# Optimization experiments

Hardware: AMD Instinct MI355X
Metric: run time of the kernel (lower is better)

Reference implementation:

```python
import jax, jax.numpy as jnp
import numpy as np

NQ = 4   # num qubits
NL = 2   # StronglyEntanglingLayers depth


def _apply_1q(state, U, w):
    # state: (B,2,2,2,2) complex64, U: (2,2) complex64, wire w in [0,NQ)
    state = jnp.moveaxis(state, w + 1, -1)
    state = jnp.einsum('ij,...j->...i', U, state)
    return jnp.moveaxis(state, -1, w + 1)


def _apply_cnot(state, cw, tw):
    # flip target axis on the control=1 slice
    s0 = jnp.take(state, jnp.array([0]), axis=cw + 1)
    s1 = jnp.take(state, jnp.array([1]), axis=cw + 1)
    s1 = jnp.flip(s1, axis=tw + 1)
    return jnp.concatenate([s0, s1], axis=cw + 1)


def _simulate(xq, qw):
    # xq: (B, NQ) angles/pi, qw: (NL, NQ, 3) Rot params
    half = 0.5 * jnp.pi * xq                      # RY(pi*x) half-angles
    c, s = jnp.cos(half), jnp.sin(half)           # (B, NQ)
    # RY on |0> gives [cos(t/2), sin(t/2)]: build product state directly
    state = jnp.stack([c[:, 0], s[:, 0]], axis=-1).astype(jnp.complex64)  # (B,2)
    for w in range(1, NQ):
        q = jnp.stack([c[:, w], s[:, w]], axis=-1).astype(jnp.complex64)
        state = jnp.einsum('b...,bj->b...j', state, q)  # -> (B,2,...,2)

    for l in range(NL):
        for w in range(NQ):
            phi, theta, omega = qw[l, w, 0], qw[l, w, 1], qw[l, w, 2]
            ct = jnp.cos(0.5 * theta)
            st = jnp.sin(0.5 * theta)
            a = 0.5 * (phi + omega)
            b = 0.5 * (phi - omega)
            # PennyLane Rot(phi,theta,omega) = RZ(omega) RY(theta) RZ(phi)
            row0 = jnp.stack([jnp.exp(-1j * a) * ct, -jnp.exp(1j * b) * st])
            row1 = jnp.stack([jnp.exp(-1j * b) * st, jnp.exp(1j * a) * ct])
            U = jnp.stack([row0, row1]).astype(jnp.complex64)
            state = _apply_1q(state, U, w)
        r = l % (NQ - 1) + 1  # default ranges of StronglyEntanglingLayers
        for w in range(NQ):
            state = _apply_cnot(state, w, (w + r) % NQ)

    p = state.real ** 2 + state.imag ** 2  # (B,2,2,2,2) probabilities
    ez = []
    for w in range(NQ):
        axes = tuple(a for a in range(1, NQ + 1) if a != w + 1)
        m = p.sum(axis=axes)               # (B,2) marginal of wire w
        ez.append(m[:, 0] - m[:, 1])       # <PauliZ>
    return jnp.stack(ez, axis=1)           # (B, NQ) float32


def setup_inputs() -> dict:
    key = jax.random.key(0)
    ks = jax.random.split(key, 6)
    N, C, H, W, OUT = 8, 128, 128, 128, 128
    x = jax.random.normal(ks[0], (N, C, H, W), dtype=jnp.float32)
    pre_w = jax.random.normal(ks[1], (NQ, C), dtype=jnp.float32) * (1.0 / np.sqrt(C))
    pre_b = jax.random.normal(ks[2], (NQ,), dtype=jnp.float32) * 0.01
    q_weights = jax.random.normal(ks[3], (NL, NQ, 3), dtype=jnp.float32)
    post_w = jax.random.normal(ks[4], (OUT, NQ), dtype=jnp.float32) * 0.5
    post_b = jax.random.normal(ks[5], (OUT,), dtype=jnp.float32) * 0.01
    return {"x": x, "pre_w": pre_w, "pre_b": pre_b, "q_weights": q_weights,
            "post_w": post_w, "post_b": post_b}


def reference(x, pre_w, pre_b, q_weights, post_w, post_b):
    N, C, H, W = x.shape
    xf = x.transpose(0, 2, 3, 1).reshape(-1, C)      # (N*H*W, C)
    xq = xf @ pre_w.T + pre_b                        # (B, NQ)
    z = _simulate(xq, q_weights)                     # (B, NQ)
    out = z @ post_w.T + post_b                      # (B, OUT)
    return out.reshape(N, H, W, -1).transpose(0, 3, 1, 2)
```

## Files before the change

kernel.cpp:

```cpp
#include <hip/hip_runtime.h>
#include <math.h>

#define NQ   4
#define NL   2
#define CD   128
#define HWSZ 16384
#define OUTC 128

typedef float f4 __attribute__((ext_vector_type(4)));

__global__ void qsetup_kernel(const float* __restrict__ qw, float* __restrict__ A) {
    __shared__ float Ur[16][17];
    __shared__ float Ui[16][17];
    __shared__ float sM[4 * 16 * 16];
    const int tid = threadIdx.x;

    if (tid < 16) {
        float sr[16], si[16];
        #pragma unroll
        for (int k = 0; k < 16; ++k) { sr[k] = (k == tid) ? 1.f : 0.f; si[k] = 0.f; }

        #pragma unroll
        for (int l = 0; l < NL; ++l) {
            #pragma unroll
            for (int w = 0; w < NQ; ++w) {
                float phi = qw[(l * NQ + w) * 3 + 0];
                float th  = qw[(l * NQ + w) * 3 + 1];
                float om  = qw[(l * NQ + w) * 3 + 2];
                float ct = __cosf(0.5f * th), st = __sinf(0.5f * th);
                float a = 0.5f * (phi + om), b = 0.5f * (phi - om);
                float sa, ca, sb, cb;
                __sincosf(a, &sa, &ca);
                __sincosf(b, &sb, &cb);
                float u00r =  ca * ct, u00i = -sa * ct;
                float u01r = -cb * st, u01i = -sb * st;
                float u10r =  cb * st, u10i = -sb * st;
                float u11r =  ca * ct, u11i =  sa * ct;
                const int wm = 1 << (3 - w);
                #pragma unroll
                for (int i = 0; i < 16; ++i) {
                    if (i & wm) continue;
                    int i1 = i | wm;
                    float a0r = sr[i],  a0i = si[i];
                    float a1r = sr[i1], a1i = si[i1];
                    sr[i]  = u00r * a0r - u00i * a0i + u01r * a1r - u01i * a1i;
                    si[i]  = u00r * a0i + u00i * a0r + u01r * a1i + u01i * a1r;
                    sr[i1] = u10r * a0r - u10i * a0i + u11r * a1r - u11i * a1i;
                    si[i1] = u10r * a0i + u10i * a0r + u11r * a1i + u11i * a1r;
                }
            }
            const int r = l % (NQ - 1) + 1;
            #pragma unroll
            for (int w = 0; w < NQ; ++w) {
                const int cm = 1 << (3 - w);
                const int tm = 1 << (3 - ((w + r) % NQ));
                #pragma unroll
                for (int i = 0; i < 16; ++i) {
                    if ((i & cm) && !(i & tm)) {
                        int i1 = i | tm;
                        float t;
                        t = sr[i]; sr[i] = sr[i1]; sr[i1] = t;
                        t = si[i]; si[i] = si[i1]; si[i1] = t;
                    }
                }
            }
        }
        #pragma unroll
        for (int k = 0; k < 16; ++k) { Ur[tid][k] = sr[k]; Ui[tid][k] = si[k]; }
    }
    __syncthreads();

    for (int t = tid; t < 4 * 16 * 16; t += blockDim.x) {
        int w = t >> 8, rem = t & 255, i = rem >> 4, j = rem & 15;
        float acc = 0.f;
        #pragma unroll
        for (int k = 0; k < 16; ++k) {
            float sgn = ((k >> (3 - w)) & 1) ? -1.f : 1.f;
            acc += sgn * (Ur[i][k] * Ur[j][k] + Ui[i][k] * Ui[j][k]);
        }
        sM[t] = acc;
    }
    __syncthreads();

    for (int t = tid; t < 4 * 81; t += blockDim.x) {
        int w = t / 81, j = t % 81;
        int j0 = j / 27, j1 = (j / 9) % 3, j2 = (j / 3) % 3, j3 = j % 3;
        int f =  ((j0 == 2) ? 8 : 0) | ((j1 == 2) ? 4 : 0)
               | ((j2 == 2) ? 2 : 0) | ((j3 == 2) ? 1 : 0);
        int zm = ((j0 == 1) ? 8 : 0) | ((j1 == 1) ? 4 : 0)
               | ((j2 == 1) ? 2 : 0) | ((j3 == 1) ? 1 : 0);
        float acc = 0.f;
        #pragma unroll
        for (int i = 0; i < 16; ++i) {
            float sgn = (__popc(i & zm) & 1) ? -1.f : 1.f;
            acc += sM[(w * 16 + (i ^ f)) * 16 + i] * sgn;
        }
        A[t] = acc * 0.0625f;
    }
}

__global__ __launch_bounds__(256) void qmain_kernel(
    const float* __restrict__ x, const float* __restrict__ pre_w,
    const float* __restrict__ pre_b, const float* __restrict__ A,
    const float* __restrict__ post_w, const float* __restrict__ post_b,
    float* __restrict__ out)
{
    __shared__ float zL[4][4][64];

    const int tid    = threadIdx.x;
    const int blk    = blockIdx.x;
    const int n      = blk >> 6;
    const int hwbase = (blk & 63) * 256;
    const float* xp  = x + (size_t)n * CD * HWSZ + hwbase + tid;

    float a0 = pre_b[0], a1 = pre_b[1], a2 = pre_b[2], a3 = pre_b[3];
    #pragma unroll
    for (int c0 = 0; c0 < CD; c0 += 32) {
        float xv[32];
        #pragma unroll
        for (int j = 0; j < 32; ++j)
            xv[j] = xp[(size_t)(c0 + j) * HWSZ];
        #pragma unroll
        for (int j = 0; j < 32; ++j) {
            const int c = c0 + j;
            a0 = fmaf(xv[j], pre_w[0 * CD + c], a0);
            a1 = fmaf(xv[j], pre_w[1 * CD + c], a1);
            a2 = fmaf(xv[j], pre_w[2 * CD + c], a2);
            a3 = fmaf(xv[j], pre_w[3 * CD + c], a3);
        }
    }

    const float PI = 3.14159265358979323846f;
    float cz0 = __cosf(PI * a0), sx0 = __sinf(PI * a0);
    float cz1 = __cosf(PI * a1), sx1 = __sinf(PI * a1);
    float cz2 = __cosf(PI * a2), sx2 = __sinf(PI * a2);
    float cz3 = __cosf(PI * a3), sx3 = __sinf(PI * a3);

    float g01[9], g23[9];
    {
        float t0[3] = { 1.f, cz0, sx0 }, t1[3] = { 1.f, cz1, sx1 };
        float t2[3] = { 1.f, cz2, sx2 }, t3[3] = { 1.f, cz3, sx3 };
        #pragma unroll
        for (int a = 0; a < 3; ++a)
            #pragma unroll
            for (int b = 0; b < 3; ++b) {
                g01[a * 3 + b] = t0[a] * t1[b];
                g23[a * 3 + b] = t2[a] * t3[b];
            }
    }

    float z0 = 0.f, z1 = 0.f, z2 = 0.f, z3 = 0.f;
    #pragma unroll
    for (int j01 = 0; j01 < 9; ++j01)
        #pragma unroll
        for (int j23 = 0; j23 < 9; ++j23) {
            float g = g01[j01] * g23[j23];
            int j = j01 * 9 + j23;
            z0 = fmaf(A[  0 + j], g, z0);
            z1 = fmaf(A[ 81 + j], g, z1);
            z2 = fmaf(A[162 + j], g, z2);
            z3 = fmaf(A[243 + j], g, z3);
        }

    zL[tid & 3][0][tid >> 2] = z0;
    zL[tid & 3][1][tid >> 2] = z1;
    zL[tid & 3][2][tid >> 2] = z2;
    zL[tid & 3][3][tid >> 2] = z3;
    __syncthreads();

    const int quad = tid & 63;
    const int og   = tid >> 6;

    float zq[4][4];
    #pragma unroll
    for (int k = 0; k < 4; ++k)
        #pragma unroll
        for (int w = 0; w < 4; ++w)
            zq[k][w] = zL[k][w][quad];

    float* op = out + (size_t)n * OUTC * HWSZ + (size_t)(og * 32) * HWSZ
                    + hwbase + quad * 4;
    #pragma unroll 8
    for (int i = 0; i < 32; ++i) {
        const int o = og * 32 + i;
        const f4 wv = *reinterpret_cast<const f4*>(&post_w[o * NQ]);
        const float bias = post_b[o];
        f4 v;
        #pragma unroll
        for (int k = 0; k < 4; ++k)
            v[k] = fmaf(zq[k][0], wv.x, fmaf(zq[k][1], wv.y,
                   fmaf(zq[k][2], wv.z, fmaf(zq[k][3], wv.w, bias))));
        __builtin_nontemporal_store(v, reinterpret_cast<f4*>(&op[(size_t)i * HWSZ]));
    }
}

extern "C" void kernel_launch(void* const* d_in, const int* in_sizes, int n_in,
                              void* d_out, int out_size, void* d_ws, size_t ws_size,
                              hipStream_t stream) {
    const float* x      = (const float*)d_in[0];
    const float* pre_w  = (const float*)d_in[1];
    const float* pre_b  = (const float*)d_in[2];
    const float* qw     = (const float*)d_in[3];
    const float* post_w = (const float*)d_in[4];
    const float* post_b = (const float*)d_in[5];
    float* out = (float*)d_out;
    float* A   = (float*)d_ws;

    hipLaunchKernelGGL(qsetup_kernel, dim3(1), dim3(256), 0, stream, qw, A);

    const int B = in_sizes[0] / CD;
    hipLaunchKernelGGL(qmain_kernel, dim3(B / 256), dim3(256), 0, stream,
                       x, pre_w, pre_b, A, post_w, post_b, out);
}
```

Before: 42.03 us.

## Stage x through LDS with 128-bit vector loads in two channel halves

Replaces the per-thread scalar strided loads of x with wide f4 global loads, where each wave loads whole channel rows. The rows are staged into a 64KB shared buffer and then read back per pixel for the pre-projection dot product. The second half of the channels is loaded into registers while the first half is being consumed. This is meant to cut the number of load instructions and improve memory-level parallelism. In exchange it uses 64KB of LDS per block, which limits occupancy, and adds several block barriers.

```diff
diff --git a/kernel.cpp b/kernel.cpp
--- a/kernel.cpp
+++ b/kernel.cpp
@@ -105,29 +105,57 @@
     const float* __restrict__ post_w, const float* __restrict__ post_b,
     float* __restrict__ out)
 {
+    __shared__ float sx[64 * 256];
     __shared__ float zL[4][4][64];
 
     const int tid    = threadIdx.x;
+    const int w      = tid >> 6;
+    const int lane   = tid & 63;
     const int blk    = blockIdx.x;
     const int n      = blk >> 6;
     const int hwbase = (blk & 63) * 256;
-    const float* xp  = x + (size_t)n * CD * HWSZ + hwbase + tid;
+    const float* xbase = x + (size_t)n * CD * HWSZ + hwbase;
 
     float a0 = pre_b[0], a1 = pre_b[1], a2 = pre_b[2], a3 = pre_b[3];
-    #pragma unroll
-    for (int c0 = 0; c0 < CD; c0 += 32) {
-        float xv[32];
-        #pragma unroll
-        for (int j = 0; j < 32; ++j)
-            xv[j] = xp[(size_t)(c0 + j) * HWSZ];
-        #pragma unroll
-        for (int j = 0; j < 32; ++j) {
-            const int c = c0 + j;
-            a0 = fmaf(xv[j], pre_w[0 * CD + c], a0);
-            a1 = fmaf(xv[j], pre_w[1 * CD + c], a1);
-            a2 = fmaf(xv[j], pre_w[2 * CD + c], a2);
-            a3 = fmaf(xv[j], pre_w[3 * CD + c], a3);
-        }
+
+    f4 xv0[16];
+    #pragma unroll
+    for (int j = 0; j < 16; ++j)
+        xv0[j] = *reinterpret_cast<const f4*>(xbase + (size_t)(j * 4 + w) * HWSZ + lane * 4);
+    #pragma unroll
+    for (int j = 0; j < 16; ++j)
+        *reinterpret_cast<f4*>(&sx[(j * 4 + w) * 256 + lane * 4]) = xv0[j];
+    __syncthreads();
+
+    f4 xv1[16];
+    #pragma unroll
+    for (int j = 0; j < 16; ++j)
+        xv1[j] = *reinterpret_cast<const f4*>(xbase + (size_t)(64 + j * 4 + w) * HWSZ + lane * 4);
+
+    #pragma unroll 16
+    for (int cc = 0; cc < 64; ++cc) {
+        const int c = cc;
+        float xs = sx[cc * 256 + tid];
+        a0 = fmaf(xs, pre_w[0 * CD + c], a0);
+        a1 = fmaf(xs, pre_w[1 * CD + c], a1);
+        a2 = fmaf(xs, pre_w[2 * CD + c], a2);
+        a3 = fmaf(xs, pre_w[3 * CD + c], a3);
+    }
+    __syncthreads();
+
+    #pragma unroll
+    for (int j = 0; j < 16; ++j)
+        *reinterpret_cast<f4*>(&sx[(j * 4 + w) * 256 + lane * 4]) = xv1[j];
+    __syncthreads();
+
+    #pragma unroll 16
+    for (int cc = 0; cc < 64; ++cc) {
+        const int c = 64 + cc;
+        float xs = sx[cc * 256 + tid];
+        a0 = fmaf(xs, pre_w[0 * CD + c], a0);
+        a1 = fmaf(xs, pre_w[1 * CD + c], a1);
+        a2 = fmaf(xs, pre_w[2 * CD + c], a2);
+        a3 = fmaf(xs, pre_w[3 * CD + c], a3);
     }
 
     const float PI = 3.14159265358979323846f;
@@ -175,8 +203,8 @@
     #pragma unroll
     for (int k = 0; k < 4; ++k)
         #pragma unroll
-        for (int w = 0; w < 4; ++w)
-            zq[k][w] = zL[k][w][quad];
+        for (int wq = 0; wq < 4; ++wq)
+            zq[k][wq] = zL[k][wq][quad];
 
     float* op = out + (size_t)n * OUTC * HWSZ + (size_t)(og * 32) * HWSZ
                     + hwbase + quad * 4;
```

Result: slower. 43.30 us (+3.0%).
